# Kernel optimization log

Measured on AMD Instinct MI355X. Metric: run time of the kernel, lower is better.

## Reference

```python
import jax, jax.numpy as jnp
import numpy as np

DIM = 512
CODEBOOK_SIZE = 2048
NUM_Q = 8
COMMIT_W = 0.25
B, T = 8, 2048


def setup_inputs() -> dict:
    key = jax.random.key(0)
    k1, k2 = jax.random.split(key)
    x = jax.random.normal(k1, (B, T, DIM), dtype=jnp.float32)
    lim = 1.0 / CODEBOOK_SIZE
    codebooks = jax.random.uniform(k2, (NUM_Q, CODEBOOK_SIZE, DIM), dtype=jnp.float32,
                                   minval=-lim, maxval=lim)
    return {"x": x, "codebooks": codebooks}


def reference(x, codebooks):
    """Residual VQ forward.
    x: (B, T, D); codebooks: (Q, K, D).
    Returns (quantized (B,T,D), indices (B,T,Q) int32, mean loss scalar).
    """
    sg = jax.lax.stop_gradient
    residual = x
    quantized = jnp.zeros_like(x)
    idx_list = []
    total_loss = jnp.zeros((), dtype=x.dtype)
    for i in range(NUM_Q):
        cb = codebooks[i]  # (K, D)
        # squared L2 distances: (B,T,K)
        d = (jnp.sum(residual * residual, axis=-1, keepdims=True)
             - 2.0 * jnp.einsum('btd,kd->btk', residual, cb)
             + jnp.sum(cb * cb, axis=-1))
        min_idx = jnp.argmin(d, axis=-1)  # (B,T)
        idx_list.append(min_idx)
        q_lvl = cb[min_idx]  # (B,T,D) gather
        quantized = quantized + q_lvl
        commit_loss = jnp.mean((sg(residual) - q_lvl) ** 2)
        codebook_loss = jnp.mean((residual - sg(q_lvl)) ** 2)
        total_loss = total_loss + commit_loss * COMMIT_W + codebook_loss
        residual = residual - sg(q_lvl)
    # straight-through estimator
    quantized = x + sg(quantized - x)
    indices = jnp.stack(idx_list, axis=-1)  # (B,T,Q)
    return quantized, indices, total_loss / NUM_Q
```

## Files before the change

### kernel.cpp

```cpp
#include <hip/hip_runtime.h>


constexpr int DIM   = 512;
constexpr int KCB   = 2048;
constexpr int NQ    = 8;
constexpr int NTOK  = 8 * 2048;
constexpr int QELEM = NTOK * DIM;
constexpr int NBLK  = KCB / 128;
constexpr float WINDOW = 1e-3f;

using short8  = __attribute__((ext_vector_type(8))) short;
using float4v = __attribute__((ext_vector_type(4))) float;

__device__ __forceinline__ unsigned short f2bf(float f) {
    unsigned u = __float_as_uint(f);
    return (unsigned short)((u + 0x7FFFu + ((u >> 16) & 1u)) >> 16);
}

__device__ __forceinline__ void gl2lds16(const void* g, void* l) {
    __builtin_amdgcn_global_load_lds(
        (__attribute__((address_space(1))) void*)g,
        (__attribute__((address_space(3))) void*)l, 16, 0, 0);
}

struct Top4 { float s[4]; int i[4]; };
__device__ __forceinline__ void t4_init(Top4& t) {
#pragma unroll
    for (int j = 0; j < 4; ++j) { t.s[j] = 3.0e38f; t.i[j] = 0x7FFFFFFF; }
}
__device__ __forceinline__ void t4_ins(Top4& t, float s, int idx) {
    if (s < t.s[3]) {
        if (s < t.s[2]) { t.s[3] = t.s[2]; t.i[3] = t.i[2];
            if (s < t.s[1]) { t.s[2] = t.s[1]; t.i[2] = t.i[1];
                if (s < t.s[0]) { t.s[1] = t.s[0]; t.i[1] = t.i[0]; t.s[0] = s; t.i[0] = idx; }
                else            { t.s[1] = s; t.i[1] = idx; }
            } else { t.s[2] = s; t.i[2] = idx; }
        } else { t.s[3] = s; t.i[3] = idx; }
    }
}

__global__ void k_initcvt(const float4* __restrict__ x, const float4* __restrict__ cbs,
                          float4* __restrict__ R, ushort4* __restrict__ Rb,
                          ushort4* __restrict__ Cbb)
{
    int i = blockIdx.x * blockDim.x + threadIdx.x;
    constexpr int N4 = QELEM / 4;
    if (i < N4) {
        float4 v = x[i];
        R[i] = v;
        Rb[i] = make_ushort4(f2bf(v.x), f2bf(v.y), f2bf(v.z), f2bf(v.w));
    } else {
        int j = i - N4;
        float4 v = cbs[j];
        Cbb[j] = make_ushort4(f2bf(v.x), f2bf(v.y), f2bf(v.z), f2bf(v.w));
    }
}

__global__ __launch_bounds__(256) void k_sqnorm_np(const float* __restrict__ A,
                                                   float* __restrict__ out)
{
#pragma clang fp contract(off)
    __shared__ float buf[4][DIM];
    __shared__ float accs[4][32];
    const int w = threadIdx.x >> 6, lane = threadIdx.x & 63;
    const int row = blockIdx.x * 4 + w;

    const float4* a4 = reinterpret_cast<const float4*>(A + (size_t)row * DIM);
    float4* b4 = reinterpret_cast<float4*>(buf[w]);
    b4[lane]      = a4[lane];
    b4[lane + 64] = a4[lane + 64];
    __syncthreads();
    if (lane < 32) {
        int blk = lane >> 3, j = lane & 7;
        const float* p = buf[w] + blk * 128 + j;
        float x0 = p[0];
        float acc = x0 * x0;
#pragma unroll
        for (int m = 1; m < 16; ++m) { float x = p[8 * m]; acc = acc + x * x; }
        accs[w][lane] = acc;
    }
    __syncthreads();
    if (lane == 0) {
        float B[4];
#pragma unroll
        for (int blk = 0; blk < 4; ++blk) {
            const float* r = &accs[w][blk * 8];
            B[blk] = ((r[0] + r[1]) + (r[2] + r[3])) + ((r[4] + r[5]) + (r[6] + r[7]));
        }
        out[row] = (B[0] + B[1]) + (B[2] + B[3]);
    }
}

__global__ __launch_bounds__(256, 4) void k_gemm_topk(
        const unsigned short* __restrict__ Rb, const unsigned short* __restrict__ Cbb,
        const float* __restrict__ c2, float* __restrict__ candS, int* __restrict__ candI)
{
    __shared__ __align__(16) char smem[34304];
    unsigned short* A0 = (unsigned short*)smem;
    unsigned short* B0 = (unsigned short*)(smem + 16384);
    float*  scb = (float*)smem;
    float*  c2s = (float*)(smem + 33792);

    const int tid  = threadIdx.x;
    const int wid  = tid >> 6, lane = tid & 63;
    const int quad = lane >> 4, l16 = lane & 15;

    const int L    = blockIdx.y * NBLK + blockIdx.x;
    const int slot = L >> 3;
    const int mb   = (L & 7) * 16 + (slot >> 4);
    const int nb   = slot & 15;

    const int tok0 = mb * 128, n0 = nb * 128;
    const int nw = (wid & 1) * 64;
    const int fbA = (wid >> 1) * 4;
    const int fbB = (wid & 1) * 4;

    if (tid < 128) c2s[tid] = c2[n0 + tid];

    float4v acc[4][4];
    float4v zero = {0.f, 0.f, 0.f, 0.f};
#pragma unroll
    for (int mi = 0; mi < 4; ++mi)
#pragma unroll
        for (int nj = 0; nj < 4; ++nj) acc[mi][nj] = zero;

    auto stage = [&](int b, int kb) {
        unsigned short* Ad = A0 + b * 4096;
        unsigned short* Bd = B0 + b * 4096;
#pragma unroll
        for (int i = 0; i < 2; ++i) {
            int mi_abs = i * 4 + wid;
            gl2lds16(&Rb[(size_t)(tok0 + mi_abs * 16 + l16) * DIM + kb + quad * 8],
                     Ad + (size_t)(i * 256 + wid * 64) * 8);
            gl2lds16(&Cbb[(size_t)(n0 + mi_abs * 16 + l16) * DIM + kb + quad * 8],
                     Bd + (size_t)(i * 256 + wid * 64) * 8);
        }
    };

    stage(0, 0);
    for (int it = 0; it < 16; ++it) {
        __syncthreads();
        if (it < 15) stage((it + 1) & 1, (it + 1) * 32);
        const unsigned short* Ac = A0 + (it & 1) * 4096;
        const unsigned short* Bc = B0 + (it & 1) * 4096;
        short8 af[4], bf[4];
#pragma unroll
        for (int mi = 0; mi < 4; ++mi)
            af[mi] = *(const short8*)(Ac + ((size_t)(fbA + mi) * 64 + lane) * 8);
#pragma unroll
        for (int nj = 0; nj < 4; ++nj)
            bf[nj] = *(const short8*)(Bc + ((size_t)(fbB + nj) * 64 + lane) * 8);
#pragma unroll
        for (int mi = 0; mi < 4; ++mi)
#pragma unroll
            for (int nj = 0; nj < 4; ++nj)
                acc[mi][nj] = __builtin_amdgcn_mfma_f32_16x16x32_bf16(
                    af[mi], bf[nj], acc[mi][nj], 0, 0, 0);
    }

    for (int h = 0; h < 2; ++h) {
        __syncthreads();
        if ((wid >> 1) == h) {
#pragma unroll
            for (int mi = 0; mi < 4; ++mi)
#pragma unroll
                for (int nj = 0; nj < 4; ++nj) {
                    int r0 = mi * 16 + quad * 4;
                    int cc = nw + nj * 16 + l16;
#pragma unroll
                    for (int e = 0; e < 4; ++e)
                        scb[(r0 + e) * 132 + cc] = acc[mi][nj][e];
                }
        }
        __syncthreads();
        int row = tid >> 2, part = tid & 3;
        Top4 t; t4_init(t);
#pragma unroll
        for (int i = 0; i < 32; ++i) {
            int col = part + 4 * i;
            float s = c2s[col] - 2.0f * scb[row * 132 + col];
            t4_ins(t, s, n0 + col);
        }
#pragma unroll
        for (int k = 1; k <= 2; k <<= 1) {
            float os[4]; int oi[4];
#pragma unroll
            for (int j = 0; j < 4; ++j) {
                os[j] = __shfl_xor(t.s[j], k, 64);
                oi[j] = __shfl_xor(t.i[j], k, 64);
            }
#pragma unroll
            for (int j = 0; j < 4; ++j) t4_ins(t, os[j], oi[j]);
        }
        if (part == 0) {
            int token = tok0 + h * 64 + row;
            size_t base = (size_t)token * 64 + (size_t)nb * 4;
#pragma unroll
            for (int j = 0; j < 4; ++j) { candS[base + j] = t.s[j]; candI[base + j] = t.i[j]; }
        }
    }
}

__global__ __launch_bounds__(256) void k_selupd(
        const float* __restrict__ candS, const int* __restrict__ candI,
        float* __restrict__ R, const float* __restrict__ cbf,
        float* __restrict__ r2, const float* __restrict__ c2,
        float* __restrict__ idx_out, float* __restrict__ partial,
        ushort4* __restrict__ Rb, const float4* __restrict__ x, int level)
{
#pragma clang fp contract(off)
    __shared__ float buf[4][DIM];
    __shared__ float accs[4][32];
    __shared__ float shl[4];
    const int w = threadIdx.x >> 6, lane = threadIdx.x & 63;
    const int t = blockIdx.x * 4 + w;
    const bool last = (level == NQ - 1);

    float sb = candS[(size_t)t * 64 + lane];
    int   ci = candI[(size_t)t * 64 + lane];
    float mn = sb;
#pragma unroll
    for (int off = 32; off; off >>= 1) mn = fminf(mn, __shfl_xor(mn, off, 64));
    unsigned long long mask = __ballot(sb <= mn + WINDOW);
    int ncand = __popcll(mask);
    int winner;
    if (ncand == 1) {
        winner = __shfl(ci, __ffsll(mask) - 1, 64);
    } else {
        int src = 0;
        if (lane < ncand) {
            unsigned long long mm = mask;
            for (int z = 0; z < lane; ++z) mm &= mm - 1;
            src = __ffsll(mm) - 1;
        }
        int cidx = __shfl(ci, src, 64);
        float s = 3.0e38f;
        int   si = 0x7FFFFFFF;
        if (lane < ncand) {
            const float* rp = R   + (size_t)t    * DIM;
            const float* cp = cbf + (size_t)cidx * DIM;
            float d = 0.f;
#pragma unroll 8
            for (int k = 0; k < DIM; ++k) d = fmaf(rp[k], cp[k], d);
            float td = 2.0f * d;
            float a  = r2[t] - td;
            s  = a + c2[cidx];
            si = cidx;
        }
#pragma unroll
        for (int off = 32; off; off >>= 1) {
            float ov = __shfl_xor(s, off, 64);
            int   oi = __shfl_xor(si, off, 64);
            if (ov < s || (ov == s && oi < si)) { s = ov; si = oi; }
        }
        winner = si;
    }
    if (lane == 0) idx_out[(size_t)t * NQ + level] = (float)winner;

    const float4* c4 = reinterpret_cast<const float4*>(cbf + (size_t)winner * DIM);
    float4*       r4 = reinterpret_cast<float4*>(R + (size_t)t * DIM);
    float4*       b4 = reinterpret_cast<float4*>(buf[w]);
    float ls = 0.f;
#pragma unroll
    for (int i = 0; i < 2; ++i) {
        int d = lane + 64 * i;
        float4 rv = r4[d], cv = c4[d];
        rv.x -= cv.x; rv.y -= cv.y; rv.z -= cv.z; rv.w -= cv.w;
        ls = ls + rv.x * rv.x; ls = ls + rv.y * rv.y;
        ls = ls + rv.z * rv.z; ls = ls + rv.w * rv.w;
        if (!last) {
            r4[d] = rv;
            b4[d] = rv;
            Rb[(size_t)t * 128 + d] = make_ushort4(f2bf(rv.x), f2bf(rv.y),
                                                   f2bf(rv.z), f2bf(rv.w));
        } else {
            float4 xv = x[(size_t)t * 128 + d];
            xv.x -= rv.x; xv.y -= rv.y; xv.z -= rv.z; xv.w -= rv.w;
            r4[d] = xv;
        }
    }

    if (!last) {
        __syncthreads();
        if (lane < 32) {
            int blk = lane >> 3, j = lane & 7;
            const float* p = buf[w] + blk * 128 + j;
            float x0 = p[0];
            float acc = x0 * x0;
#pragma unroll
            for (int m = 1; m < 16; ++m) { float xx = p[8 * m]; acc = acc + xx * xx; }
            accs[w][lane] = acc;
        }
        __syncthreads();
        if (lane == 0) {
            float B[4];
#pragma unroll
            for (int blk = 0; blk < 4; ++blk) {
                const float* r = &accs[w][blk * 8];
                B[blk] = ((r[0] + r[1]) + (r[2] + r[3])) + ((r[4] + r[5]) + (r[6] + r[7]));
            }
            r2[t] = (B[0] + B[1]) + (B[2] + B[3]);
        }
    }

#pragma unroll
    for (int off = 32; off; off >>= 1) ls += __shfl_down(ls, off, 64);
    if (lane == 0) shl[w] = ls;
    __syncthreads();
    if (threadIdx.x == 0) partial[blockIdx.x] = (shl[0] + shl[1]) + (shl[2] + shl[3]);
}

__global__ __launch_bounds__(256) void k_finalize_loss(const float* __restrict__ partial,
                                                       float* __restrict__ loss_out)
{
    double s = 0.0;
    for (int i = threadIdx.x; i < NQ * (NTOK / 4); i += 256) s += (double)partial[i];
#pragma unroll
    for (int off = 32; off; off >>= 1) s += __shfl_down(s, off, 64);
    __shared__ double sh[4];
    if ((threadIdx.x & 63) == 0) sh[threadIdx.x >> 6] = s;
    __syncthreads();
    if (threadIdx.x == 0) {
        double tot = (sh[0] + sh[1]) + (sh[2] + sh[3]);
        loss_out[0] = (float)(tot * 1.25 / ((double)NQ * (double)QELEM));
    }
}

extern "C" void kernel_launch(void* const* d_in, const int* in_sizes, int n_in,
                              void* d_out, int out_size, void* d_ws, size_t ws_size,
                              hipStream_t stream)
{
    const float* x   = (const float*)d_in[0];
    const float* cbs = (const float*)d_in[1];

    float* qout     = (float*)d_out;
    float* idx_out  = qout + QELEM;
    float* loss_out = idx_out + (size_t)NTOK * NQ;
    float* R        = qout;

    char* ws = (char*)d_ws;
    size_t off = 0;
    unsigned short* Rb   = (unsigned short*)(ws + off); off += (size_t)QELEM * 2;
    unsigned short* Cbb  = (unsigned short*)(ws + off); off += (size_t)QELEM * 2;
    float*          c2   = (float*)(ws + off);          off += (size_t)NQ * KCB * 4;
    float*          r2   = (float*)(ws + off);          off += (size_t)NTOK * 4;
    float*          part = (float*)(ws + off);          off += (size_t)NQ * (NTOK / 4) * 4;
    float*          candS= (float*)(ws + off);          off += (size_t)NTOK * 64 * 4;
    int*            candI= (int*)(ws + off);            off += (size_t)NTOK * 64 * 4;

    k_initcvt<<<2 * (QELEM / 4) / 256, 256, 0, stream>>>((const float4*)x, (const float4*)cbs,
                                                         (float4*)R, (ushort4*)Rb,
                                                         (ushort4*)Cbb);
    k_sqnorm_np<<<NQ * KCB / 4, 256, 0, stream>>>(cbs, c2);
    k_sqnorm_np<<<NTOK / 4, 256, 0, stream>>>(R, r2);

    for (int q = 0; q < NQ; ++q) {
        const float*          cbq  = cbs + (size_t)q * KCB * DIM;
        const unsigned short* cbbq = Cbb + (size_t)q * KCB * DIM;
        const float*          c2q  = c2 + (size_t)q * KCB;
        dim3 g(NBLK, NTOK / 128);
        k_gemm_topk<<<g, 256, 0, stream>>>(Rb, cbbq, c2q, candS, candI);
        k_selupd<<<NTOK / 4, 256, 0, stream>>>(candS, candI, R, cbq, r2, c2q,
                                               idx_out, part + (size_t)q * (NTOK / 4),
                                               (ushort4*)Rb, (const float4*)x, q);
    }

    k_finalize_loss<<<1, 256, 0, stream>>>(part, loss_out);
}
```

Measured before the change: 1.223 ms.

## Triple-buffer GEMM LDS pipeline and stage residual in LDS for candidate rescoring

The GEMM top-k kernel moves from double to triple buffering of the A/B tiles in shared memory. It uses explicit vmcnt waits and raw barriers so two tile loads stay in flight while the MFMAs run, and lowers launch bounds from 4 to 3 blocks per SM to fit the larger LDS footprint. The select/update kernel loads the residual row once into registers and shared memory. It then rescores candidates with float4 reads from LDS instead of scalar global reads, and reuses the register copy for the update. The risk is lower occupancy and fragile hand-written waitcnt logic.

```diff
diff --git a/kernel.cpp b/kernel.cpp
--- a/kernel.cpp
+++ b/kernel.cpp
@@ -91,15 +91,15 @@
     }
 }
 
-__global__ __launch_bounds__(256, 4) void k_gemm_topk(
+__global__ __launch_bounds__(256, 3) void k_gemm_topk(
         const unsigned short* __restrict__ Rb, const unsigned short* __restrict__ Cbb,
         const float* __restrict__ c2, float* __restrict__ candS, int* __restrict__ candI)
 {
-    __shared__ __align__(16) char smem[34304];
+    __shared__ __align__(16) char smem[49664];
     unsigned short* A0 = (unsigned short*)smem;
-    unsigned short* B0 = (unsigned short*)(smem + 16384);
+    unsigned short* B0 = (unsigned short*)(smem + 24576);
     float*  scb = (float*)smem;
-    float*  c2s = (float*)(smem + 33792);
+    float*  c2s = (float*)(smem + 49152);
 
     const int tid  = threadIdx.x;
     const int wid  = tid >> 6, lane = tid & 63;
@@ -137,12 +137,9 @@
         }
     };
 
-    stage(0, 0);
-    for (int it = 0; it < 16; ++it) {
-        __syncthreads();
-        if (it < 15) stage((it + 1) & 1, (it + 1) * 32);
-        const unsigned short* Ac = A0 + (it & 1) * 4096;
-        const unsigned short* Bc = B0 + (it & 1) * 4096;
+    auto compute = [&](int b) {
+        const unsigned short* Ac = A0 + b * 4096;
+        const unsigned short* Bc = B0 + b * 4096;
         short8 af[4], bf[4];
 #pragma unroll
         for (int mi = 0; mi < 4; ++mi)
@@ -156,7 +153,24 @@
             for (int nj = 0; nj < 4; ++nj)
                 acc[mi][nj] = __builtin_amdgcn_mfma_f32_16x16x32_bf16(
                     af[mi], bf[nj], acc[mi][nj], 0, 0, 0);
-    }
+    };
+
+    stage(0, 0);
+    stage(1, 32);
+    int cur = 0, pf = 2;
+    for (int it = 0; it < 15; ++it) {
+        asm volatile("s_waitcnt vmcnt(4)" ::: "memory");
+        __builtin_amdgcn_s_barrier();
+        __builtin_amdgcn_sched_barrier(0);
+        if (it < 14) stage(pf, (it + 2) * 32);
+        compute(cur);
+        cur = (cur == 2) ? 0 : cur + 1;
+        pf  = (pf  == 2) ? 0 : pf  + 1;
+    }
+    asm volatile("s_waitcnt vmcnt(0)" ::: "memory");
+    __builtin_amdgcn_s_barrier();
+    __builtin_amdgcn_sched_barrier(0);
+    compute(cur);
 
     for (int h = 0; h < 2; ++h) {
         __syncthreads();
@@ -215,6 +229,12 @@
     const int w = threadIdx.x >> 6, lane = threadIdx.x & 63;
     const int t = blockIdx.x * 4 + w;
     const bool last = (level == NQ - 1);
+
+    float4* r4 = reinterpret_cast<float4*>(R + (size_t)t * DIM);
+    float4* b4 = reinterpret_cast<float4*>(buf[w]);
+    float4 rr[2];
+    rr[0] = r4[lane];      rr[1] = r4[lane + 64];
+    b4[lane] = rr[0];      b4[lane + 64] = rr[1];
 
     float sb = candS[(size_t)t * 64 + lane];
     int   ci = candI[(size_t)t * 64 + lane];
@@ -237,11 +257,18 @@
         float s = 3.0e38f;
         int   si = 0x7FFFFFFF;
         if (lane < ncand) {
-            const float* rp = R   + (size_t)t    * DIM;
-            const float* cp = cbf + (size_t)cidx * DIM;
+            const float4* cp4 = reinterpret_cast<const float4*>(cbf + (size_t)cidx * DIM);
+            const float4* rp4 = reinterpret_cast<const float4*>(buf[w]);
             float d = 0.f;
-#pragma unroll 8
-            for (int k = 0; k < DIM; ++k) d = fmaf(rp[k], cp[k], d);
+#pragma unroll 4
+            for (int j = 0; j < DIM / 4; ++j) {
+                float4 cv = cp4[j];
+                float4 rv = rp4[j];
+                d = fmaf(rv.x, cv.x, d);
+                d = fmaf(rv.y, cv.y, d);
+                d = fmaf(rv.z, cv.z, d);
+                d = fmaf(rv.w, cv.w, d);
+            }
             float td = 2.0f * d;
             float a  = r2[t] - td;
             s  = a + c2[cidx];
@@ -258,13 +285,11 @@
     if (lane == 0) idx_out[(size_t)t * NQ + level] = (float)winner;
 
     const float4* c4 = reinterpret_cast<const float4*>(cbf + (size_t)winner * DIM);
-    float4*       r4 = reinterpret_cast<float4*>(R + (size_t)t * DIM);
-    float4*       b4 = reinterpret_cast<float4*>(buf[w]);
     float ls = 0.f;
 #pragma unroll
     for (int i = 0; i < 2; ++i) {
         int d = lane + 64 * i;
-        float4 rv = r4[d], cv = c4[d];
+        float4 rv = rr[i], cv = c4[d];
         rv.x -= cv.x; rv.y -= cv.y; rv.z -= cv.z; rv.w -= cv.w;
         ls = ls + rv.x * rv.x; ls = ls + rv.y * rv.y;
         ls = ls + rv.z * rv.z; ls = ls + rv.w * rv.w;
```

After: 1.041 ms. -14.8%, faster.
